# Kernel optimization log

Hardware: AMD Instinct MI355X
Metric: run time of the kernel (lower is better)

The kernel has to match this reference:

```python
import jax, jax.numpy as jnp
import numpy as np

R, C, B, E, H = 16, 256, 12, 768, 12  # rows, cols, batch(==heads, see notes), embed, heads
D = E // H
NUM_BUCKETS, MAX_DISTANCE = 32, 50000


def _relative_position_bucket(distances):
    # T5-style log-spaced buckets, matching the torch code (trunc toward zero).
    n = jnp.abs(distances)
    max_exact = NUM_BUCKETS // 2
    is_small = n < max_exact
    nf = jnp.maximum(n.astype(jnp.float32), 1.0)  # guard log(0); masked by is_small
    val_large = max_exact + (
        jnp.log(nf / max_exact) / np.log(MAX_DISTANCE / max_exact) * (NUM_BUCKETS - max_exact - 1)
    ).astype(jnp.int32)
    val_large = jnp.minimum(val_large, NUM_BUCKETS - 1)
    return jnp.where(is_small, n.astype(jnp.int32), val_large)


def setup_inputs() -> dict:
    key = jax.random.key(0)
    ks = jax.random.split(key, 11)
    s = 1.0 / np.sqrt(E)
    x = jax.random.normal(ks[0], (R, C, B, E), jnp.float32)
    distances = jax.random.randint(ks[1], (B, C, C), 0, MAX_DISTANCE, jnp.int32)
    Wq = jax.random.normal(ks[2], (E, E), jnp.float32) * s
    bq = jnp.zeros((E,), jnp.float32)
    Wk = jax.random.normal(ks[3], (E, E), jnp.float32) * s
    bk = jnp.zeros((E,), jnp.float32)
    Wv = jax.random.normal(ks[4], (E, E), jnp.float32) * s
    bv = jnp.zeros((E,), jnp.float32)
    Wo = jax.random.normal(ks[5], (E, E), jnp.float32) * s
    bo = jnp.zeros((E,), jnp.float32)
    rel_bias = jax.random.normal(ks[6], (NUM_BUCKETS, H), jnp.float32) * 0.02
    return dict(x=x, distances=distances, Wq=Wq, bq=bq, Wk=Wk, bk=bk,
                Wv=Wv, bv=bv, Wo=Wo, bo=bo, rel_bias=rel_bias)


def reference(x, distances, Wq, bq, Wk, bk, Wv, bv, Wo, bo, rel_bias):
    scaling = (D ** -0.5) / np.sqrt(R)  # align_scaling: head_dim^-0.5 / sqrt(num_rows)
    q = (x @ Wq.T + bq).reshape(R, C, B, H, D) * scaling
    k = (x @ Wk.T + bk).reshape(R, C, B, H, D)
    # row-aggregated scores: sum over rows r -> (h, n, i, j)
    attn = jnp.einsum('rinhd,rjnhd->hnij', q, k)
    # relative position bias: (n, i, j) -> buckets -> (n, i, j, h) -> (n, h, i, j)
    buckets = _relative_position_bucket(distances)
    bias = jnp.transpose(rel_bias[buckets], (0, 3, 1, 2))
    # NOTE: source adds (n,h,i,j) bias onto (h,n,i,j) scores positionally; valid since B == H.
    attn = attn + bias
    probs = jax.nn.softmax(attn, axis=-1)  # (h, n, i, j)
    v = (x @ Wv.T + bv).reshape(R, C, B, H, D)
    ctx = jnp.einsum('hnij,rjnhd->rinhd', probs, v).reshape(R, C, B, E)
    out = ctx @ Wo.T + bo
    return out, probs
```

## Files before the change

### kernel.cpp

```cpp
#include <hip/hip_runtime.h>
#include <stdint.h>
#include <math.h>

#define R_ 16
#define C_ 256
#define B_ 12
#define E_ 768
#define H_ 12
#define D_ 64
#define TOK (R_*C_*B_)
#define HALF_TOK 24576

#define VT_N_ELEMS 3145728
#define CTX_N_ELEMS 3145728
#define QK_HALF 37748736

typedef __bf16 bf16x8 __attribute__((ext_vector_type(8)));
typedef float floatx4 __attribute__((ext_vector_type(4)));

__device__ __forceinline__ unsigned short f2bf(float f) {
    union { unsigned int i; float f; } v; v.f = f;
    unsigned int i = v.i;
    return (unsigned short)((i + 0x7fffu + ((i >> 16) & 1u)) >> 16);
}
__device__ __forceinline__ bf16x8 cvt8(floatx4 lo, floatx4 hi) {
    bf16x8 r;
    r[0] = (__bf16)lo[0]; r[1] = (__bf16)lo[1]; r[2] = (__bf16)lo[2]; r[3] = (__bf16)lo[3];
    r[4] = (__bf16)hi[0]; r[5] = (__bf16)hi[1]; r[6] = (__bf16)hi[2]; r[7] = (__bf16)hi[3];
    return r;
}
__device__ __forceinline__ void gload16(const unsigned short* g, unsigned short* l) {
    __builtin_amdgcn_global_load_lds(
        (const __attribute__((address_space(1))) unsigned int*)g,
        (__attribute__((address_space(3))) unsigned int*)l, 16, 0, 0);
}

template<int MODE>
__device__ __forceinline__ void gemm_body(const void* __restrict__ Ap,
                                          const void* __restrict__ Btp,
                                          const float* __restrict__ bias,
                                          void* __restrict__ Cout,
                                          int nBase, int rbx, int rby, int rbz,
                                          unsigned short* As, unsigned short* Bs)
{
    constexpr bool AGL = (MODE == 0 || MODE == 4);
    constexpr int K = (MODE == 2) ? 256 : 768;
    constexpr int kIters = K >> 5;
    constexpr int GX = (MODE==0) ? 12 : (MODE==2) ? 8 : 6;
    constexpr int GY = (MODE==0) ? 192 : (MODE==2) ? 2 : 32;
    constexpr int GZ = (MODE==0) ? 1 : (MODE==2) ? 24 : 2;

    const int tid  = threadIdx.x;
    const int wave = tid >> 6, lane = tid & 63;
    const int quad = lane >> 4, l15 = lane & 15;
    const int wr = wave >> 1, wc = wave & 1;

    const int lin = (rbz * GY + rby) * GX + rbx;
    const int tt  = (lin & 7) * ((GX * GY * GZ) >> 3) + (lin >> 3);
    const int bx  = tt % GX;
    const int rem = tt / GX;
    const int by  = rem % GY, bz = rem / GY;
    const int row0 = by * 128, col0 = bx * 128;

    int hIdx = 0, nn = 0, nIdx = 0;
    if (MODE == 2) { hIdx = bz % 12; nn = bz / 12; nIdx = nBase + nn; }
    if (MODE == 3 || MODE == 4) { nn = bz; nIdx = nBase + nn; }

    const int rA0 = tid >> 2;
    const int ck  = tid & 3;
    const int sw  = (tid >> 3) & 3;
    const int kko = ((ck ^ sw) << 3);

    const unsigned short* Bt = (const unsigned short*)Btp;
    const unsigned short *gB0, *gB1;
    if (MODE == 2) {
        gB0 = Bt + (((size_t)nn * 12 + hIdx) * 1024 + col0 + rA0) * 256 + kko;
        gB1 = Bt + (((size_t)nn * 12 + hIdx) * 1024 + col0 + rA0 + 64) * 256 + kko;
    } else {
        gB0 = Bt + (size_t)(col0 + rA0) * 768 + kko;
        gB1 = Bt + (size_t)(col0 + rA0 + 64) * 768 + kko;
    }

    const unsigned short* gA0u = nullptr; const unsigned short* gA1u = nullptr;
    const float* gA0f = nullptr; const float* gA1f = nullptr;
    if (MODE == 0) {
        gA0u = (const unsigned short*)Ap + (size_t)(row0 + rA0) * 768 + kko;
        gA1u = (const unsigned short*)Ap + (size_t)(row0 + rA0 + 64) * 768 + kko;
    } else if (MODE == 4) {
        gA0u = (const unsigned short*)Ap + (size_t)nn * CTX_N_ELEMS
               + (size_t)(row0 + rA0) * 768 + kko;
        gA1u = (const unsigned short*)Ap + (size_t)nn * CTX_N_ELEMS
               + (size_t)(row0 + rA0 + 64) * 768 + kko;
    } else if (MODE == 3) {
        gA0f = (const float*)Ap + ((size_t)(row0 + rA0) * 12 + nIdx) * 768 + kko;
        gA1f = (const float*)Ap + ((size_t)(row0 + rA0 + 64) * 12 + nIdx) * 768 + kko;
    } else {
        gA0f = (const float*)Ap + ((size_t)(hIdx * 12 + nIdx)) * 65536
               + (size_t)(row0 + rA0) * 256 + kko;
        gA1f = (const float*)Ap + ((size_t)(hIdx * 12 + nIdx)) * 65536
               + (size_t)(row0 + rA0 + 64) * 256 + kko;
    }

    unsigned short* lA0 = As + wave * 512;
    unsigned short* lA1 = As + 2048 + wave * 512;
    unsigned short* lB0 = Bs + wave * 512;
    unsigned short* lB1 = Bs + 2048 + wave * 512;

    const floatx4 zero = {0.f, 0.f, 0.f, 0.f};
    floatx4 acc[4][4];
#pragma unroll
    for (int i = 0; i < 4; ++i)
#pragma unroll
        for (int j = 0; j < 4; ++j) acc[i][j] = zero;

    const int chO = ((quad ^ ((l15 >> 1) & 3)) << 3);

    floatx4 u0l = zero, u0h = zero, u1l = zero, u1h = zero;
    floatx4 p0l = zero, p0h = zero, p1l = zero, p1h = zero;
    if (!AGL) {
        u0l = *(const floatx4*)(gA0f);     u0h = *(const floatx4*)(gA0f + 4);
        u1l = *(const floatx4*)(gA1f);     u1h = *(const floatx4*)(gA1f + 4);
    }

#define GSTEP(KT, UL0, UH0, UL1, UH1, PL0, PH0, PL1, PH1)                         \
    {                                                                              \
        __syncthreads();                                \
        gload16(gB0 + (KT) * 32, lB0);                                             \
        gload16(gB1 + (KT) * 32, lB1);                                             \
        if (AGL) {                                                                 \
            gload16(gA0u + (KT) * 32, lA0);                                        \
            gload16(gA1u + (KT) * 32, lA1);                                        \
        } else {                                                                   \
            *(bf16x8*)(As + tid * 8)        = cvt8(UL0, UH0);                      \
            *(bf16x8*)(As + 2048 + tid * 8) = cvt8(UL1, UH1);                      \
        }                                                                          \
        __syncthreads();                                      \
        if (!AGL && ((KT) + 1 < kIters)) {             \
            PL0 = *(const floatx4*)(gA0f + ((KT) + 1) * 32);                       \
            PH0 = *(const floatx4*)(gA0f + ((KT) + 1) * 32 + 4);                   \
            PL1 = *(const floatx4*)(gA1f + ((KT) + 1) * 32);                       \
            PH1 = *(const floatx4*)(gA1f + ((KT) + 1) * 32 + 4);                   \
        }                                                                          \
        bf16x8 af[4], bfr[4];                                                      \
        _Pragma("unroll")                                                          \
        for (int t = 0; t < 4; ++t) {                                              \
            af[t]  = *(const bf16x8*)(As + (wr * 64 + t * 16 + l15) * 32 + chO);   \
            bfr[t] = *(const bf16x8*)(Bs + (wc * 64 + t * 16 + l15) * 32 + chO);   \
        }                                                                          \
        _Pragma("unroll")                                                          \
        for (int tm = 0; tm < 4; ++tm)                                             \
            _Pragma("unroll")                                                      \
            for (int tn = 0; tn < 4; ++tn)                                         \
                acc[tm][tn] = __builtin_amdgcn_mfma_f32_16x16x32_bf16(             \
                    af[tm], bfr[tn], acc[tm][tn], 0, 0, 0);                        \
    }

    for (int kt = 0; kt < kIters; kt += 2) {
        GSTEP(kt,     u0l, u0h, u1l, u1h, p0l, p0h, p1l, p1h);
        GSTEP(kt + 1, p0l, p0h, p1l, p1h, u0l, u0h, u1l, u1h);
    }
#undef GSTEP

#pragma unroll
    for (int tm = 0; tm < 4; ++tm) {
        const int rbase = row0 + wr * 64 + tm * 16 + quad * 4;
#pragma unroll
        for (int tn = 0; tn < 4; ++tn) {
            const int cc = col0 + wc * 64 + tn * 16 + l15;
#pragma unroll
            for (int rr = 0; rr < 4; ++rr) {
                float vv = acc[tm][tn][rr];
                const int rowg = rbase + rr;
                if (MODE == 0) {
                    const int tg = nBase * HALF_TOK + rowg;
                    const int m = tg / 12, n = tg - m * 12;
                    const int r = m >> 8, i = m & 255;
                    const int sel = cc >= 768 ? 1 : 0;
                    const int ccl = cc - sel * 768;
                    const int h = ccl >> 6, d = ccl & 63;
                    ((unsigned short*)Cout)[(size_t)sel * QK_HALF
                        + ((size_t)(n * 12 + h) * 256 + i) * 1024 + r * 64 + d]
                        = f2bf(vv + bias[cc]);
                } else if (MODE == 2) {
                    ((unsigned short*)Cout)[(size_t)nn * CTX_N_ELEMS
                        + (((size_t)(cc >> 6)) * 256 + rowg) * 768
                        + hIdx * 64 + (cc & 63)] = f2bf(vv);
                } else if (MODE == 3) {
                    ((unsigned short*)Cout)[(size_t)nn * VT_N_ELEMS
                        + (((size_t)(cc >> 6)) * 1024
                           + (rowg >> 8) * 64 + (cc & 63)) * 256
                        + (rowg & 255)] = f2bf(vv + bias[cc]);
                } else {
                    ((float*)Cout)[((size_t)rowg * 12 + nIdx) * 768 + cc] = vv + bias[cc];
                }
            }
        }
    }
}

template<int MODE>
__global__ __launch_bounds__(256)
void gemm_bt(const void* __restrict__ Ap,
             const void* __restrict__ Btp,
             const float* __restrict__ bias,
             void* __restrict__ Cout,
             int nBase)
{
    __shared__ __align__(16) unsigned short As[128 * 32];
    __shared__ __align__(16) unsigned short Bs[128 * 32];
    gemm_body<MODE>(Ap, Btp, bias, Cout, nBase,
                    blockIdx.x, blockIdx.y, blockIdx.z, As, Bs);
}

__global__ __launch_bounds__(256)
void fused_vo(const float* __restrict__ x, const unsigned short* __restrict__ wv,
              const float* __restrict__ bv, unsigned short* __restrict__ vt,
              const unsigned short* __restrict__ ctx,
              const unsigned short* __restrict__ wo,
              const float* __restrict__ bo, float* __restrict__ outp,
              int cV, int cO)
{
    __shared__ __align__(16) unsigned short As[128 * 32];
    __shared__ __align__(16) unsigned short Bs[128 * 32];
    if (blockIdx.z < 2)
        gemm_body<3>(x, wv, bv, vt, cV, blockIdx.x, blockIdx.y, blockIdx.z, As, Bs);
    else
        gemm_body<4>(ctx, wo, bo, outp, cO, blockIdx.x, blockIdx.y,
                     blockIdx.z - 2, As, Bs);
}

__global__ __launch_bounds__(512)
void scores_sm(const unsigned short* __restrict__ q,
               const unsigned short* __restrict__ k,
               const int* __restrict__ buckets,
               const float* __restrict__ rb,
               float* __restrict__ probs)
{
    __shared__ __align__(16) unsigned short As[128 * 32];
    __shared__ __align__(16) unsigned short Bs[256 * 32];

    const int tid  = threadIdx.x;
    const int w    = tid >> 6, lane = tid & 63;
    const int quad = lane >> 4, l15 = lane & 15;

    const int lin = (int)blockIdx.z * 2 + (int)blockIdx.y;
    const int tt  = (lin & 7) * 36 + (lin >> 3);
    const int by  = tt % 2, bz = tt / 2;
    const int row0 = by * 128;
    const int h = bz % 12, n = bz / 12;

    const int rA0 = tid >> 2;
    const int ck  = tid & 3;
    const int sw  = (tid >> 3) & 3;
    const int kko = ((ck ^ sw) << 3);

    const unsigned short* gA  = q + ((size_t)bz * 256 + row0 + rA0) * 1024 + kko;
    const unsigned short* gB0 = k + ((size_t)bz * 256 + rA0) * 1024 + kko;
    const unsigned short* gB1 = k + ((size_t)bz * 256 + rA0 + 128) * 1024 + kko;

    unsigned short* lA  = As + w * 512;
    unsigned short* lB0 = Bs + w * 512;
    unsigned short* lB1 = Bs + 4096 + w * 512;

    const floatx4 zero = {0.f, 0.f, 0.f, 0.f};
    floatx4 acc[16];
#pragma unroll
    for (int t = 0; t < 16; ++t) acc[t] = zero;

    const int chO = ((quad ^ ((l15 >> 1) & 3)) << 3);

    for (int kt = 0; kt < 32; ++kt) {
        __syncthreads();
        gload16(gA  + kt * 32, lA);
        gload16(gB0 + kt * 32, lB0);
        gload16(gB1 + kt * 32, lB1);
        __syncthreads();
        const bf16x8 af = *(const bf16x8*)(As + (w * 16 + l15) * 32 + chO);
#pragma unroll
        for (int tn = 0; tn < 16; ++tn) {
            const bf16x8 bfr = *(const bf16x8*)(Bs + (tn * 16 + l15) * 32 + chO);
            acc[tn] = __builtin_amdgcn_mfma_f32_16x16x32_bf16(af, bfr, acc[tn], 0, 0, 0);
        }
    }

    const int i0 = row0 + w * 16 + quad * 4;
    float mx[4] = {-3.4e38f, -3.4e38f, -3.4e38f, -3.4e38f};
#pragma unroll
    for (int tn = 0; tn < 16; ++tn) {
        const int j = tn * 16 + l15;
#pragma unroll
        for (int rr = 0; rr < 4; ++rr) {
            const int bkt = buckets[((size_t)h * 256 + i0 + rr) * 256 + j];
            const float s = acc[tn][rr] * 0.03125f + rb[bkt * 12 + n];
            acc[tn][rr] = s;
            mx[rr] = fmaxf(mx[rr], s);
        }
    }
#pragma unroll
    for (int rr = 0; rr < 4; ++rr)
#pragma unroll
        for (int off = 1; off < 16; off <<= 1)
            mx[rr] = fmaxf(mx[rr], __shfl_xor(mx[rr], off, 64));
    float sm[4] = {0.f, 0.f, 0.f, 0.f};
#pragma unroll
    for (int tn = 0; tn < 16; ++tn)
#pragma unroll
        for (int rr = 0; rr < 4; ++rr) {
            const float e = expf(acc[tn][rr] - mx[rr]);
            acc[tn][rr] = e;
            sm[rr] += e;
        }
#pragma unroll
    for (int rr = 0; rr < 4; ++rr)
#pragma unroll
        for (int off = 1; off < 16; off <<= 1)
            sm[rr] += __shfl_xor(sm[rr], off, 64);
    float inv[4];
#pragma unroll
    for (int rr = 0; rr < 4; ++rr) inv[rr] = 1.f / sm[rr];

    float* prow = probs + ((size_t)(h * 12 + n)) * 65536;
#pragma unroll
    for (int tn = 0; tn < 16; ++tn) {
        const int j = tn * 16 + l15;
#pragma unroll
        for (int rr = 0; rr < 4; ++rr)
            prow[(size_t)(i0 + rr) * 256 + j] = acc[tn][rr] * inv[rr];
    }
}

__global__ __launch_bounds__(256)
void cvt_bulk(const float* __restrict__ src, unsigned short* __restrict__ dst, int n)
{
    const int i = (blockIdx.x * 256 + threadIdx.x) * 8;
    if (i >= n) return;
    floatx4 a = ((const floatx4*)(src + i))[0];
    floatx4 b = ((const floatx4*)(src + i))[1];
    *(bf16x8*)(dst + i) = cvt8(a, b);
}

__global__ __launch_bounds__(256)
void cvt_weights(const float* __restrict__ Wq, const float* __restrict__ Wk,
                 const float* __restrict__ Wv, const float* __restrict__ Wo,
                 const float* __restrict__ bq, const float* __restrict__ bk,
                 unsigned short* __restrict__ wqk, unsigned short* __restrict__ wvb,
                 unsigned short* __restrict__ wob, float* __restrict__ bqk)
{
    const int gid = blockIdx.x * 256 + threadIdx.x;
    const int W8 = 73728;
    if (gid < 4 * W8) {
        const int sec = gid / W8, off = (gid - sec * W8) * 8;
        const float* src = (sec == 0) ? Wq : (sec == 1) ? Wk : (sec == 2) ? Wv : Wo;
        unsigned short* dst = (sec == 0) ? wqk : (sec == 1) ? (wqk + 589824)
                              : (sec == 2) ? wvb : wob;
        floatx4 a = ((const floatx4*)(src + off))[0];
        floatx4 b = ((const floatx4*)(src + off))[1];
        *(bf16x8*)(dst + off) = cvt8(a, b);
    } else {
        const int b = gid - 4 * W8;
        if (b < 1536) bqk[b] = (b < 768) ? bq[b] : bk[b - 768];
    }
}

__global__ __launch_bounds__(256)
void bucket_kernel(const int* __restrict__ dist, int* __restrict__ buckets)
{
    const int idx = blockIdx.x * 256 + threadIdx.x;
    if (idx >= B_ * C_ * C_) return;
    const int dv = dist[idx];
    const int n = dv < 0 ? -dv : dv;
    int bkt;
    if (n < 16) {
        bkt = n;
    } else {
        const float lg = logf((float)n * 0.0625f);
        const float t  = (lg / 8.047189562170502f) * 15.0f;
        bkt = 16 + (int)t;
        if (bkt > 31) bkt = 31;
    }
    buckets[idx] = bkt;
}

extern "C" void kernel_launch(void* const* d_in, const int* in_sizes, int n_in,
                              void* d_out, int out_size, void* d_ws, size_t ws_size,
                              hipStream_t stream)
{
    const float* x    = (const float*)d_in[0];
    const int*   dist = (const int*)d_in[1];
    const float* Wq   = (const float*)d_in[2];
    const float* bq   = (const float*)d_in[3];
    const float* Wk   = (const float*)d_in[4];
    const float* bk   = (const float*)d_in[5];
    const float* Wv   = (const float*)d_in[6];
    const float* bv   = (const float*)d_in[7];
    const float* Wo   = (const float*)d_in[8];
    const float* bo   = (const float*)d_in[9];
    const float* rb   = (const float*)d_in[10];

    float* outp  = (float*)d_out;
    float* probs = (float*)d_out + (size_t)TOK * E_;

    unsigned short* qs   = (unsigned short*)d_out;
    unsigned short* ks   = (unsigned short*)d_out + QK_HALF;
    unsigned short* x_bf = (unsigned short*)probs;

    char* ws = (char*)d_ws;
    unsigned short* wo_bf  = (unsigned short*)(ws);
    unsigned short* wv_bf  = (unsigned short*)(ws + 1179648);
    float*          bqk    = (float*)(ws + 2359296);
    unsigned short* wqk_bf = (unsigned short*)(ws + 2365440);
    int*            buckets= (int*)(ws + 4724736);
    unsigned short* vt     = (unsigned short*)(ws + 2365440);
    unsigned short* ctx    = (unsigned short*)(ws + 14948352);

    dim3 blk(256);

    cvt_weights<<<dim3(1158), blk, 0, stream>>>(Wq, Wk, Wv, Wo, bq, bk,
                                                wqk_bf, wv_bf, wo_bf, bqk);
    bucket_kernel<<<dim3(3072), blk, 0, stream>>>(dist, buckets);

    for (int half = 0; half < 2; ++half) {
        cvt_bulk<<<dim3(9216), blk, 0, stream>>>(
            x + (size_t)half * HALF_TOK * 768, x_bf, HALF_TOK * 768);
        gemm_bt<0><<<dim3(12, 192), blk, 0, stream>>>(x_bf, wqk_bf, bqk, qs, half);
    }

    scores_sm<<<dim3(1, 2, 144), dim3(512), 0, stream>>>(qs, ks, buckets, rb, probs);

    gemm_bt<3><<<dim3(6, 32, 2), blk, 0, stream>>>(x, wv_bf, bv, vt, 0);
    gemm_bt<2><<<dim3(8, 2, 24), blk, 0, stream>>>(probs, vt, nullptr, ctx, 0);
    for (int k = 1; k < 6; ++k) {
        fused_vo<<<dim3(6, 32, 4), blk, 0, stream>>>(
            x, wv_bf, bv, vt, ctx, wo_bf, bo, outp, 2 * k, 2 * (k - 1));
        gemm_bt<2><<<dim3(8, 2, 24), blk, 0, stream>>>(probs, vt, nullptr, ctx, 2 * k);
    }
    gemm_bt<4><<<dim3(6, 32, 2), blk, 0, stream>>>(ctx, wo_bf, bo, outp, 10);
}
```

Measured before the change: 872.4 us.

## Restructure V/ctx/output pipeline into full-batch V GEMM and row-quarter chunks

Rewrites the value and output projection schedule. x is converted once to bf16 into the output buffer, V is computed in a single large GEMM written transposed into that buffer, then ctx and the output projection run in four row-quarter chunks instead of six per-batch-pair fused launches. The bucket and weight-convert kernels are also merged into one prep launch. The intent is fewer launches, bf16 A loads for the V GEMM, and bigger grids. The cost is an extra full-size bf16 conversion pass and a different ctx workspace layout.

Measured after the change: 941.7 us. +7.9%, slower.

```diff
diff --git a/kernel.cpp b/kernel.cpp
--- a/kernel.cpp
+++ b/kernel.cpp
@@ -11,9 +11,10 @@
 #define TOK (R_*C_*B_)
 #define HALF_TOK 24576
 
-#define VT_N_ELEMS 3145728
-#define CTX_N_ELEMS 3145728
 #define QK_HALF 37748736
+#define VT_BASE 37748736
+#define VT_QUARTER 9437184
+#define CTXQ_ELEMS 9437184
 
 typedef __bf16 bf16x8 __attribute__((ext_vector_type(8)));
 typedef float floatx4 __attribute__((ext_vector_type(4)));
@@ -36,35 +37,37 @@
 }
 
 template<int MODE>
-__device__ __forceinline__ void gemm_body(const void* __restrict__ Ap,
-                                          const void* __restrict__ Btp,
-                                          const float* __restrict__ bias,
-                                          void* __restrict__ Cout,
-                                          int nBase, int rbx, int rby, int rbz,
-                                          unsigned short* As, unsigned short* Bs)
+__global__ __launch_bounds__(256)
+void gemm_bt(const void* __restrict__ Ap,
+             const void* __restrict__ Btp,
+             const float* __restrict__ bias,
+             void* __restrict__ Cout,
+             int nBase)
 {
-    constexpr bool AGL = (MODE == 0 || MODE == 4);
+    __shared__ __align__(16) unsigned short As[128 * 32];
+    __shared__ __align__(16) unsigned short Bs[128 * 32];
+
+    constexpr bool AGL = (MODE != 2);
     constexpr int K = (MODE == 2) ? 256 : 768;
     constexpr int kIters = K >> 5;
-    constexpr int GX = (MODE==0) ? 12 : (MODE==2) ? 8 : 6;
-    constexpr int GY = (MODE==0) ? 192 : (MODE==2) ? 2 : 32;
-    constexpr int GZ = (MODE==0) ? 1 : (MODE==2) ? 24 : 2;
+    constexpr int GX = (MODE==0) ? 12 : (MODE==2) ? 2 : (MODE==3) ? 6 : 6;
+    constexpr int GY = (MODE==0) ? 192 : (MODE==2) ? 2 : (MODE==3) ? 384 : 96;
+    constexpr int GZ = (MODE==2) ? 144 : 1;
 
     const int tid  = threadIdx.x;
     const int wave = tid >> 6, lane = tid & 63;
     const int quad = lane >> 4, l15 = lane & 15;
     const int wr = wave >> 1, wc = wave & 1;
 
-    const int lin = (rbz * GY + rby) * GX + rbx;
+    const int lin = ((int)blockIdx.z * GY + (int)blockIdx.y) * GX + (int)blockIdx.x;
     const int tt  = (lin & 7) * ((GX * GY * GZ) >> 3) + (lin >> 3);
     const int bx  = tt % GX;
     const int rem = tt / GX;
     const int by  = rem % GY, bz = rem / GY;
     const int row0 = by * 128, col0 = bx * 128;
 
-    int hIdx = 0, nn = 0, nIdx = 0;
-    if (MODE == 2) { hIdx = bz % 12; nn = bz / 12; nIdx = nBase + nn; }
-    if (MODE == 3 || MODE == 4) { nn = bz; nIdx = nBase + nn; }
+    int hIdx = 0, nIdx = 0;
+    if (MODE == 2) { hIdx = bz % 12; nIdx = bz / 12; }
 
     const int rA0 = tid >> 2;
     const int ck  = tid & 3;
@@ -74,8 +77,10 @@
     const unsigned short* Bt = (const unsigned short*)Btp;
     const unsigned short *gB0, *gB1;
     if (MODE == 2) {
-        gB0 = Bt + (((size_t)nn * 12 + hIdx) * 1024 + col0 + rA0) * 256 + kko;
-        gB1 = Bt + (((size_t)nn * 12 + hIdx) * 1024 + col0 + rA0 + 64) * 256 + kko;
+        const size_t vq = VT_BASE + (size_t)nBase * VT_QUARTER
+                          + ((size_t)(nIdx * 12 + hIdx) * 256) * 256;
+        gB0 = Bt + vq + (size_t)(col0 + rA0) * 256 + kko;
+        gB1 = Bt + vq + (size_t)(col0 + rA0 + 64) * 256 + kko;
     } else {
         gB0 = Bt + (size_t)(col0 + rA0) * 768 + kko;
         gB1 = Bt + (size_t)(col0 + rA0 + 64) * 768 + kko;
@@ -83,17 +88,9 @@
 
     const unsigned short* gA0u = nullptr; const unsigned short* gA1u = nullptr;
     const float* gA0f = nullptr; const float* gA1f = nullptr;
-    if (MODE == 0) {
+    if (AGL) {
         gA0u = (const unsigned short*)Ap + (size_t)(row0 + rA0) * 768 + kko;
         gA1u = (const unsigned short*)Ap + (size_t)(row0 + rA0 + 64) * 768 + kko;
-    } else if (MODE == 4) {
-        gA0u = (const unsigned short*)Ap + (size_t)nn * CTX_N_ELEMS
-               + (size_t)(row0 + rA0) * 768 + kko;
-        gA1u = (const unsigned short*)Ap + (size_t)nn * CTX_N_ELEMS
-               + (size_t)(row0 + rA0 + 64) * 768 + kko;
-    } else if (MODE == 3) {
-        gA0f = (const float*)Ap + ((size_t)(row0 + rA0) * 12 + nIdx) * 768 + kko;
-        gA1f = (const float*)Ap + ((size_t)(row0 + rA0 + 64) * 12 + nIdx) * 768 + kko;
     } else {
         gA0f = (const float*)Ap + ((size_t)(hIdx * 12 + nIdx)) * 65536
                + (size_t)(row0 + rA0) * 256 + kko;
@@ -182,51 +179,22 @@
                         + ((size_t)(n * 12 + h) * 256 + i) * 1024 + r * 64 + d]
                         = f2bf(vv + bias[cc]);
                 } else if (MODE == 2) {
-                    ((unsigned short*)Cout)[(size_t)nn * CTX_N_ELEMS
-                        + (((size_t)(cc >> 6)) * 256 + rowg) * 768
-                        + hIdx * 64 + (cc & 63)] = f2bf(vv);
+                    ((unsigned short*)Cout)[((((size_t)(cc >> 6)) * 256 + rowg) * 12
+                        + nIdx) * 768 + hIdx * 64 + (cc & 63)] = f2bf(vv);
                 } else if (MODE == 3) {
-                    ((unsigned short*)Cout)[(size_t)nn * VT_N_ELEMS
-                        + (((size_t)(cc >> 6)) * 1024
-                           + (rowg >> 8) * 64 + (cc & 63)) * 256
-                        + (rowg & 255)] = f2bf(vv + bias[cc]);
+                    const int m = rowg / 12, n = rowg - m * 12;
+                    const int r = m >> 8, j = m & 255;
+                    const int h = cc >> 6, d = cc & 63;
+                    ((unsigned short*)Cout)[VT_BASE + (size_t)(r >> 2) * VT_QUARTER
+                        + ((size_t)(n * 12 + h) * 256 + (r & 3) * 64 + d) * 256 + j]
+                        = f2bf(vv + bias[cc]);
                 } else {
-                    ((float*)Cout)[((size_t)rowg * 12 + nIdx) * 768 + cc] = vv + bias[cc];
+                    ((float*)Cout)[((size_t)(nBase * 12288 + rowg)) * 768 + cc]
+                        = vv + bias[cc];
                 }
             }
         }
     }
-}
-
-template<int MODE>
-__global__ __launch_bounds__(256)
-void gemm_bt(const void* __restrict__ Ap,
-             const void* __restrict__ Btp,
-             const float* __restrict__ bias,
-             void* __restrict__ Cout,
-             int nBase)
-{
-    __shared__ __align__(16) unsigned short As[128 * 32];
-    __shared__ __align__(16) unsigned short Bs[128 * 32];
-    gemm_body<MODE>(Ap, Btp, bias, Cout, nBase,
-                    blockIdx.x, blockIdx.y, blockIdx.z, As, Bs);
-}
-
-__global__ __launch_bounds__(256)
-void fused_vo(const float* __restrict__ x, const unsigned short* __restrict__ wv,
-              const float* __restrict__ bv, unsigned short* __restrict__ vt,
-              const unsigned short* __restrict__ ctx,
-              const unsigned short* __restrict__ wo,
-              const float* __restrict__ bo, float* __restrict__ outp,
-              int cV, int cO)
-{
-    __shared__ __align__(16) unsigned short As[128 * 32];
-    __shared__ __align__(16) unsigned short Bs[128 * 32];
-    if (blockIdx.z < 2)
-        gemm_body<3>(x, wv, bv, vt, cV, blockIdx.x, blockIdx.y, blockIdx.z, As, Bs);
-    else
-        gemm_body<4>(ctx, wo, bo, outp, cO, blockIdx.x, blockIdx.y,
-                     blockIdx.z - 2, As, Bs);
 }
 
 __global__ __launch_bounds__(512)
@@ -340,13 +308,31 @@
 }
 
 __global__ __launch_bounds__(256)
-void cvt_weights(const float* __restrict__ Wq, const float* __restrict__ Wk,
-                 const float* __restrict__ Wv, const float* __restrict__ Wo,
-                 const float* __restrict__ bq, const float* __restrict__ bk,
-                 unsigned short* __restrict__ wqk, unsigned short* __restrict__ wvb,
-                 unsigned short* __restrict__ wob, float* __restrict__ bqk)
+void prep(const int* __restrict__ dist, int* __restrict__ buckets,
+          const float* __restrict__ Wq, const float* __restrict__ Wk,
+          const float* __restrict__ Wv, const float* __restrict__ Wo,
+          const float* __restrict__ bq, const float* __restrict__ bk,
+          unsigned short* __restrict__ wqk, unsigned short* __restrict__ wvb,
+          unsigned short* __restrict__ wob, float* __restrict__ bqk)
 {
-    const int gid = blockIdx.x * 256 + threadIdx.x;
+    if (blockIdx.x < 3072) {
+        const int idx = blockIdx.x * 256 + threadIdx.x;
+        if (idx >= B_ * C_ * C_) return;
+        const int dv = dist[idx];
+        const int n = dv < 0 ? -dv : dv;
+        int bkt;
+        if (n < 16) {
+            bkt = n;
+        } else {
+            const float lg = logf((float)n * 0.0625f);
+            const float t  = (lg / 8.047189562170502f) * 15.0f;
+            bkt = 16 + (int)t;
+            if (bkt > 31) bkt = 31;
+        }
+        buckets[idx] = bkt;
+        return;
+    }
+    const int gid = (blockIdx.x - 3072) * 256 + threadIdx.x;
     const int W8 = 73728;
     if (gid < 4 * W8) {
         const int sec = gid / W8, off = (gid - sec * W8) * 8;
@@ -360,25 +346,6 @@
         const int b = gid - 4 * W8;
         if (b < 1536) bqk[b] = (b < 768) ? bq[b] : bk[b - 768];
     }
-}
-
-__global__ __launch_bounds__(256)
-void bucket_kernel(const int* __restrict__ dist, int* __restrict__ buckets)
-{
-    const int idx = blockIdx.x * 256 + threadIdx.x;
-    if (idx >= B_ * C_ * C_) return;
-    const int dv = dist[idx];
-    const int n = dv < 0 ? -dv : dv;
-    int bkt;
-    if (n < 16) {
-        bkt = n;
-    } else {
-        const float lg = logf((float)n * 0.0625f);
-        const float t  = (lg / 8.047189562170502f) * 15.0f;
-        bkt = 16 + (int)t;
-        if (bkt > 31) bkt = 31;
-    }
-    buckets[idx] = bkt;
 }
 
 extern "C" void kernel_launch(void* const* d_in, const int* in_sizes, int n_in,
@@ -400,24 +367,23 @@
     float* outp  = (float*)d_out;
     float* probs = (float*)d_out + (size_t)TOK * E_;
 
-    unsigned short* qs   = (unsigned short*)d_out;
-    unsigned short* ks   = (unsigned short*)d_out + QK_HALF;
+    unsigned short* dob  = (unsigned short*)d_out;
+    unsigned short* qs   = dob;
+    unsigned short* ks   = dob + QK_HALF;
     unsigned short* x_bf = (unsigned short*)probs;
 
     char* ws = (char*)d_ws;
     unsigned short* wo_bf  = (unsigned short*)(ws);
     unsigned short* wv_bf  = (unsigned short*)(ws + 1179648);
     float*          bqk    = (float*)(ws + 2359296);
-    unsigned short* wqk_bf = (unsigned short*)(ws + 2365440);
-    int*            buckets= (int*)(ws + 4724736);
-    unsigned short* vt     = (unsigned short*)(ws + 2365440);
-    unsigned short* ctx    = (unsigned short*)(ws + 14948352);
+    unsigned short* ctx_q  = (unsigned short*)(ws + 2365440);
+    int*            buckets= (int*)(ws + 21239808);
+    unsigned short* wqk_bf = (unsigned short*)(ws + 24385536);
 
     dim3 blk(256);
 
-    cvt_weights<<<dim3(1158), blk, 0, stream>>>(Wq, Wk, Wv, Wo, bq, bk,
-                                                wqk_bf, wv_bf, wo_bf, bqk);
-    bucket_kernel<<<dim3(3072), blk, 0, stream>>>(dist, buckets);
+    prep<<<dim3(4230), blk, 0, stream>>>(dist, buckets, Wq, Wk, Wv, Wo, bq, bk,
+                                         wqk_bf, wv_bf, wo_bf, bqk);
 
     for (int half = 0; half < 2; ++half) {
         cvt_bulk<<<dim3(9216), blk, 0, stream>>>(
@@ -427,12 +393,10 @@
 
     scores_sm<<<dim3(1, 2, 144), dim3(512), 0, stream>>>(qs, ks, buckets, rb, probs);
 
-    gemm_bt<3><<<dim3(6, 32, 2), blk, 0, stream>>>(x, wv_bf, bv, vt, 0);
-    gemm_bt<2><<<dim3(8, 2, 24), blk, 0, stream>>>(probs, vt, nullptr, ctx, 0);
-    for (int k = 1; k < 6; ++k) {
-        fused_vo<<<dim3(6, 32, 4), blk, 0, stream>>>(
-            x, wv_bf, bv, vt, ctx, wo_bf, bo, outp, 2 * k, 2 * (k - 1));
-        gemm_bt<2><<<dim3(8, 2, 24), blk, 0, stream>>>(probs, vt, nullptr, ctx, 2 * k);
-    }
-    gemm_bt<4><<<dim3(6, 32, 2), blk, 0, stream>>>(ctx, wo_bf, bo, outp, 10);
-}
+    cvt_bulk<<<dim3(18432), blk, 0, stream>>>(x, dob, TOK * E_);
+    gemm_bt<3><<<dim3(6, 384), blk, 0, stream>>>(dob, wv_bf, bv, dob, 0);
+    for (int q = 0; q < 4; ++q) {
+        gemm_bt<2><<<dim3(2, 2, 144), blk, 0, stream>>>(probs, dob, nullptr, ctx_q, q);
+        gemm_bt<4><<<dim3(6, 96), blk, 0, stream>>>(ctx_q, wo_bf, bo, outp, q);
+    }
+}
```
